# Optimization experiments

Measured on AMD Instinct MI355X. Metric: run time of the kernel, lower is better.

## Reference

```python
import jax, jax.numpy as jnp
import numpy as np


def setup_inputs() -> dict:
    key = jax.random.key(0)
    k_x, k_q, k_k, k_v = jax.random.split(key, 4)
    B, S, E, D = 4, 2048, 1024, 1024
    scale = 1.0 / np.sqrt(E)
    return {
        "x": jax.random.normal(k_x, (B, S, E), dtype=jnp.float32),
        # nn.Linear weight matrices, shape [out_dim, in_dim]; y = x @ W.T
        "w_q": jax.random.normal(k_q, (D, E), dtype=jnp.float32) * scale,
        "w_k": jax.random.normal(k_k, (D, E), dtype=jnp.float32) * scale,
        "w_v": jax.random.normal(k_v, (D, E), dtype=jnp.float32) * scale,
    }


def reference(x, w_q, w_k, w_v):
    # x: [B, S, E]; w_*: [D, E] (torch nn.Linear convention)
    B, S, E = x.shape
    q = jnp.einsum("bse,de->bsd", x, w_q)  # [B, S, D]
    k = jnp.einsum("bse,de->bsd", x, w_k)
    v = jnp.einsum("bse,de->bsd", x, w_v)
    D = q.shape[-1]
    # raw scores, then causal mask (strictly upper triangle -> -inf), then
    # scale by 1/sqrt(D) inside softmax exactly as the original does.
    scores = jnp.einsum("bsd,btd->bst", q, k)  # [B, S, S]
    causal = jnp.tril(jnp.ones((S, S), dtype=bool))  # True = keep
    scores = jnp.where(causal[None], scores, -jnp.inf)
    attn = jax.nn.softmax(scores / jnp.sqrt(jnp.asarray(D, x.dtype)), axis=-1)
    # dropout p=0.0 -> identity
    return jnp.einsum("bst,btd->bsd", attn, v)  # [B, S, D]
```

## Files before the change

kernel.cpp:

```cpp
#include <hip/hip_runtime.h>
#include <hip/hip_bf16.h>


typedef unsigned short u16;
typedef __attribute__((ext_vector_type(4))) u16   u16x4;
typedef __attribute__((ext_vector_type(8))) u16   u16x8;
typedef __attribute__((ext_vector_type(8))) short short8;
typedef __attribute__((ext_vector_type(4))) float f32x4;
typedef __attribute__((ext_vector_type(4))) int   i32x4;

__device__ inline u16 f2b(float v) {
    __hip_bfloat16 b = __float2bfloat16(v);
    return *reinterpret_cast<u16*>(&b);
}
__device__ inline float b2f(u16 v) {
    unsigned int u = ((unsigned int)v) << 16;
    return *reinterpret_cast<float*>(&u);
}

template <typename T> __device__ inline void store_elem(T* p, float v);
template <> __device__ inline void store_elem<float>(float* p, float v) { *p = v; }
template <> __device__ inline void store_elem<u16>(u16* p, float v)     { *p = f2b(v); }

__device__ inline void gload_lds16(const u16* g, u16* l) {
    __builtin_amdgcn_global_load_lds(
        (const __attribute__((address_space(1))) void*)g,
        (__attribute__((address_space(3))) void*)l, 16, 0, 0);
}

__global__ __launch_bounds__(256) void cast_all_kernel(
    const float* __restrict__ x,  const float* __restrict__ wq,
    const float* __restrict__ wk, const float* __restrict__ wv,
    u16* __restrict__ dst) {
    int q = blockIdx.x * 256 + threadIdx.x;
    const float* src;
    int sidx;
    if (q < 2097152) { src = x; sidx = q * 4; }
    else {
        int qq = q - 2097152;
        int w  = qq >> 18;
        sidx   = (qq & 262143) * 4;
        src    = (w == 0) ? wq : (w == 1) ? wk : wv;
    }
    float4 v = *(const float4*)(src + sidx);
    u16x4 o;
    o.x = f2b(v.x); o.y = f2b(v.y); o.z = f2b(v.z); o.w = f2b(v.w);
    *(u16x4*)(dst + q * 4) = o;
}

#define MT 128
#define NT 128
#define BKH 32
#define HSZ (MT * BKH)

template <int TRANS, typename OutT>
__device__ __forceinline__ void gemm_core(
    u16* __restrict__ As, u16* __restrict__ Bs,
    const u16* __restrict__ Ab, int lda,
    const u16* __restrict__ Bb, int ldb,
    OutT* __restrict__ Cb, int ldc,
    int m0, int n0, int kbeg, int kend)
{
    const int tid  = threadIdx.x;
    const int lane = tid & 63;
    const int wave = tid >> 6;
    const int quad = lane >> 4;
    const int r16  = lane & 15;
    const int mw   = (wave >> 1) * 64;
    const int nw   = (wave & 1) * 64;

    const int c0 = tid, c1 = tid + 256;
    const int r0 = c0 >> 2, k0 = (c0 & 3) * 8;
    const int r1 = c1 >> 2, k1 = (c1 & 3) * 8;
    const int oa0 = (m0 + r0) * lda + k0;
    const int oa1 = (m0 + r1) * lda + k1;
    const int ob0 = (n0 + r0) * ldb + k0;
    const int ob1 = (n0 + r1) * ldb + k1;

    f32x4 acc[4][4] = {};

    for (int kk = kbeg; kk < kend; kk += 2 * BKH) {
        __syncthreads();
        gload_lds16(Ab + (kk + oa0),        &As[c0 * 8]);
        gload_lds16(Ab + (kk + oa1),        &As[c1 * 8]);
        gload_lds16(Ab + (kk + BKH + oa0),  &As[HSZ + c0 * 8]);
        gload_lds16(Ab + (kk + BKH + oa1),  &As[HSZ + c1 * 8]);
        gload_lds16(Bb + (kk + ob0),        &Bs[c0 * 8]);
        gload_lds16(Bb + (kk + ob1),        &Bs[c1 * 8]);
        gload_lds16(Bb + (kk + BKH + ob0),  &Bs[HSZ + c0 * 8]);
        gload_lds16(Bb + (kk + BKH + ob1),  &Bs[HSZ + c1 * 8]);
        __syncthreads();

#pragma unroll
        for (int h = 0; h < 2; h++) {
            short8 af[4], bf[4];
#pragma unroll
            for (int i = 0; i < 4; i++)
                af[i] = *(const short8*)&As[h * HSZ + (mw + i * 16 + r16) * BKH + quad * 8];
#pragma unroll
            for (int j = 0; j < 4; j++)
                bf[j] = *(const short8*)&Bs[h * HSZ + (nw + j * 16 + r16) * BKH + quad * 8];
#pragma unroll
            for (int i = 0; i < 4; i++)
#pragma unroll
                for (int j = 0; j < 4; j++)
                    acc[i][j] = __builtin_amdgcn_mfma_f32_16x16x32_bf16(af[i], bf[j], acc[i][j], 0, 0, 0);
        }
    }

    if (TRANS == 0) {
#pragma unroll
        for (int i = 0; i < 4; i++)
#pragma unroll
            for (int j = 0; j < 4; j++)
#pragma unroll
                for (int r = 0; r < 4; r++) {
                    int m = m0 + mw + i * 16 + quad * 4 + r;
                    int n = n0 + nw + j * 16 + r16;
                    store_elem(&Cb[(long long)m * ldc + n], acc[i][j][r]);
                }
    } else {
#pragma unroll
        for (int i = 0; i < 4; i++)
#pragma unroll
            for (int j = 0; j < 4; j++) {
                int mbase = m0 + mw + i * 16 + quad * 4;
                int d     = n0 + nw + j * 16 + r16;
                int b     = mbase >> 11;
                int s     = mbase & 2047;
                u16x4 o;
#pragma unroll
                for (int r = 0; r < 4; r++) o[r] = f2b(acc[i][j][r]);
                *(u16x4*)((u16*)Cb + (((b << 10) + d) * 2048 + s)) = o;
            }
    }
}

__global__ __launch_bounds__(256, 4) void gemm_qkv(
    const u16* __restrict__ xb, const u16* __restrict__ wb,
    u16* __restrict__ qk, u16* __restrict__ vt) {
    __shared__ __align__(16) u16 As[2 * HSZ];
    __shared__ __align__(16) u16 Bs[2 * HSZ];
    int bx = blockIdx.x, m0 = blockIdx.y * MT;
    if (bx < 16)
        gemm_core<0, u16>(As, Bs, xb, 1024, wb, 1024, qk, 2048,
                          m0, bx * 128, 0, 1024);
    else
        gemm_core<1, u16>(As, Bs, xb, 1024, wb + 2048 * 1024, 1024, vt, 2048,
                          m0, (bx - 16) * 128, 0, 1024);
}

__global__ __launch_bounds__(256, 4) void gemm_scores(
    const u16* __restrict__ qk, u16* __restrict__ sc) {
    __shared__ __align__(16) u16 As[2 * HSZ];
    __shared__ __align__(16) u16 Bs[2 * HSZ];
    int t = blockIdx.x;
    float ff = sqrtf(8.0f * t + 1.0f);
    int m = (int)((ff - 1.0f) * 0.5f);
    while ((m + 1) * (m + 2) / 2 <= t) m++;
    while (m * (m + 1) / 2 > t) m--;
    int m0 = m * MT;
    int n0 = (t - m * (m + 1) / 2) * NT;
    const u16* Ab = qk + (long long)blockIdx.z * 2048 * 2048;
    const u16* Bb = Ab + 1024;
    u16* Cb = sc + (long long)blockIdx.z * 2048 * 2048;
    gemm_core<0, u16>(As, Bs, Ab, 2048, Bb, 2048, Cb, 2048, m0, n0, 0, 1024);
}

__global__ __launch_bounds__(256, 4) void gemm_pv(
    const u16* __restrict__ P, const u16* __restrict__ vt,
    float* __restrict__ out, float* __restrict__ part)
{
    __shared__ __align__(16) u16 As[2 * HSZ];
    __shared__ __align__(16) u16 Bs[2 * HSZ];
    const int bid = blockIdx.x;
    int m, chunk, n;
    if (bid < 80) {
        int q = bid >> 3; n = bid & 7;
        if (q < 9) { m = 7 + q; chunk = 0; } else { m = 15; chunk = 1; }
    } else {
        int r = bid - 80; int s = 7 - (r >> 4); int t = r & 15;
        n = t & 7;
        if (t < 8) { m = s - 1; chunk = 0; } else { m = s + 7; chunk = 1; }
    }
    const int m0 = m * MT, n0 = n * NT;
    const int kbeg = chunk ? 1024 : 0;
    const int kend = chunk ? (m0 + MT) : min(1024, m0 + MT);
    const int b = blockIdx.z;

    const u16* Ab = P  + (long long)b * 2048 * 2048;
    const u16* Bb = vt + (long long)b * 1024 * 2048;
    float* Cb = (chunk == 0)
        ? out  + (long long)b * 2097152
        : part + (long long)b * 1048576 - 1024LL * 1024;
    gemm_core<0, float>(As, Bs, Ab, 2048, Bb, 2048, Cb, 1024, m0, n0, kbeg, kend);
}

__global__ __launch_bounds__(256) void pv_combine(float* __restrict__ out,
                                                  const float* __restrict__ part) {
    long long idx = ((long long)blockIdx.x * 256 + threadIdx.x) * 8;
    long long bb = idx >> 20;
    long long j  = idx & 1048575;
    float* o = out + bb * 2097152 + 1048576 + j;
    const float* p = part + bb * 1048576 + j;
    float4 o0 = *(float4*)o, o1 = *(float4*)(o + 4);
    float4 p0 = *(const float4*)p, p1 = *(const float4*)(p + 4);
    o0.x += p0.x; o0.y += p0.y; o0.z += p0.z; o0.w += p0.w;
    o1.x += p1.x; o1.y += p1.y; o1.z += p1.z; o1.w += p1.w;
    *(float4*)o = o0; *(float4*)(o + 4) = o1;
}

__global__ __launch_bounds__(256) void softmax_kernel(const u16* __restrict__ sc,
                                                      u16* __restrict__ P) {
    const int S = 2048;
    int row = blockIdx.x;
    int i   = row & (S - 1);
    int n   = i + 1;
    int kendr = (i & ~127) + 128;
    const u16* srow = sc + (long long)row * S;
    u16*       prow = P  + (long long)row * S;

    int j0 = threadIdx.x * 8;
    u16x8 raw = {};
    if (j0 <= i) raw = *(const u16x8*)(srow + j0);
    float v[8];
#pragma unroll
    for (int e = 0; e < 8; e++) v[e] = (j0 + e < n) ? b2f(raw[e]) : -1e30f;

    __shared__ float red[8];
    float lmax = v[0];
#pragma unroll
    for (int e = 1; e < 8; e++) lmax = fmaxf(lmax, v[e]);
    for (int o = 32; o > 0; o >>= 1) lmax = fmaxf(lmax, __shfl_xor(lmax, o, 64));
    int wid = threadIdx.x >> 6;
    if ((threadIdx.x & 63) == 0) red[wid] = lmax;
    __syncthreads();
    float Mx = fmaxf(fmaxf(red[0], red[1]), fmaxf(red[2], red[3]));

    const float C = 0.045112384f;
    float ev[8];
    float lsum = 0.f;
#pragma unroll
    for (int e = 0; e < 8; e++) {
        ev[e] = (j0 + e < n) ? exp2f((v[e] - Mx) * C) : 0.f;
        lsum += ev[e];
    }
    for (int o = 32; o > 0; o >>= 1) lsum += __shfl_xor(lsum, o, 64);
    if ((threadIdx.x & 63) == 0) red[4 + wid] = lsum;
    __syncthreads();
    float inv = 1.0f / (red[4] + red[5] + red[6] + red[7]);

    if (j0 < kendr) {
        u16x8 o8;
#pragma unroll
        for (int e = 0; e < 8; e++) o8[e] = f2b(ev[e] * inv);
        *(u16x8*)(prow + j0) = o8;
    }
}

extern "C" void kernel_launch(void* const* d_in, const int* in_sizes, int n_in,
                              void* d_out, int out_size, void* d_ws, size_t ws_size,
                              hipStream_t stream) {
    const float* x  = (const float*)d_in[0];
    const float* wq = (const float*)d_in[1];
    const float* wk = (const float*)d_in[2];
    const float* wv = (const float*)d_in[3];
    float* out = (float*)d_out;

    char* ws = (char*)d_ws;
    u16*   xb   = (u16*)(ws);
    u16*   wb   = (u16*)(ws + 16777216LL);
    u16*   qk   = (u16*)(ws + 23068672LL);
    u16*   sc   = (u16*)(ws + 56623104LL);
    u16*   P    = (u16*)(ws + 90177536LL);
    u16*   vt   = (u16*)(ws + 123731968LL);
    float* part = (float*)(ws + 140509184LL);

    cast_all_kernel<<<11264, 256, 0, stream>>>(x, wq, wk, wv, xb);

    gemm_qkv<<<dim3(24, 64, 1), 256, 0, stream>>>(xb, wb, qk, vt);

    gemm_scores<<<dim3(136, 1, 4), 256, 0, stream>>>(qk, sc);

    softmax_kernel<<<8192, 256, 0, stream>>>(sc, P);

    gemm_pv<<<dim3(192, 1, 4), 256, 0, stream>>>(P, vt, out, part);
    pv_combine<<<2048, 256, 0, stream>>>(out, part);
}
```

Baseline: 243.3 us.

## Replace QKV projection GEMM with 256x256-tile 8-wave pipelined kernel

Replaces the 128x128-tile QKV projection GEMM with a dedicated 256x256-tile kernel using 512 threads, a BK=64 double-buffered LDS pipeline with XOR-swizzled layout, interleaved prefetch between MFMA phases, s_setprio hints, and a block-index swizzle for L2 locality. The larger tile increases arithmetic intensity and reduces global/LDS traffic per FLOP. It trades this for fewer blocks (384) and higher register and LDS pressure, with hand-tuned waitcnt and barriers that must be exactly right.

```diff
diff --git a/kernel.cpp b/kernel.cpp
--- a/kernel.cpp
+++ b/kernel.cpp
@@ -46,6 +46,188 @@
     u16x4 o;
     o.x = f2b(v.x); o.y = f2b(v.y); o.z = f2b(v.z); o.w = f2b(v.w);
     *(u16x4*)(dst + q * 4) = o;
+}
+
+__global__ __launch_bounds__(512) void gemm_qkv256(
+    const u16* __restrict__ xb, const u16* __restrict__ wb,
+    u16* __restrict__ qk, u16* __restrict__ vt)
+{
+    __shared__ __align__(16) u16 lds[2][2][16384];
+
+    const int tid  = threadIdx.x;
+    const int lane = tid & 63;
+    const int wave = tid >> 6;
+    const int quad = lane >> 4;
+    const int r16  = lane & 15;
+    const int wm   = wave >> 2;
+    const int wn   = wave & 3;
+
+    int flat = blockIdx.x;
+    int swz  = (flat & 7) * 48 + (flat >> 3);
+    int bx   = swz % 12;
+    int m0   = (swz / 12) * 256;
+    const bool isV = (bx >= 8);
+    const int  n0  = (isV ? bx - 8 : bx) * 256;
+    const u16* __restrict__ Ab = xb;
+    const u16* __restrict__ Bb = wb + (isV ? 2048 * 1024 : 0);
+
+    int gA[2][2], gB[2][2], lA[2][2], lB[2][2];
+    {
+        const int cswz = ((lane & 3) * 8) ^ (((lane >> 5) & 1) << 4);
+        const int rsub = lane >> 2;
+#pragma unroll
+        for (int u = 0; u < 2; ++u)
+#pragma unroll
+            for (int j = 0; j < 2; ++j) {
+                int s   = j * 8 + wave;
+                int sh  = s >> 1, cg = s & 1;
+                int rgA = (sh & 3) + (sh >> 2) * 8 + u * 4;
+                int rgB = sh + u * 8;
+                int cl  = cg * 32 + cswz;
+                gA[u][j] = (m0 + rgA * 16 + rsub) * 1024 + cl;
+                gB[u][j] = (n0 + rgB * 16 + rsub) * 1024 + cl;
+                lA[u][j] = (rgA * 2 + cg) * 512 + lane * 8;
+                lB[u][j] = (rgB * 2 + cg) * 512 + lane * 8;
+            }
+    }
+
+#define STAGE_A(BUF, U, KK) do { \
+        gload_lds16(Ab + gA[U][0] + (KK), &lds[BUF][0][lA[U][0]]); \
+        gload_lds16(Ab + gA[U][1] + (KK), &lds[BUF][0][lA[U][1]]); } while (0)
+#define STAGE_B(BUF, U, KK) do { \
+        gload_lds16(Bb + gB[U][0] + (KK), &lds[BUF][1][lB[U][0]]); \
+        gload_lds16(Bb + gB[U][1] + (KK), &lds[BUF][1][lB[U][1]]); } while (0)
+
+    const int cswr = (quad * 8) ^ ((r16 >> 3) << 4);
+    const int rdA0 = wm * 16 * 512 + r16 * 32 + cswr;
+    const int rdB0 = wn * 8  * 512 + r16 * 32 + cswr;
+
+    f32x4 acc[8][4] = {};
+
+    STAGE_B(0, 0, 0);  STAGE_B(0, 1, 0);  STAGE_A(0, 0, 0);  STAGE_A(0, 1, 0);
+    STAGE_B(1, 0, 64); STAGE_B(1, 1, 64); STAGE_A(1, 0, 64); STAGE_A(1, 1, 64);
+    asm volatile("s_waitcnt vmcnt(8)" ::: "memory");
+    __builtin_amdgcn_s_barrier();
+
+    for (int t = 0; t < 16; ++t) {
+        const int  buf = t & 1;
+        const int  kk2 = t * 64 + 128;
+        const bool pf  = (t < 14);
+        const u16* Al  = lds[buf][0];
+        const u16* Bl  = lds[buf][1];
+        short8 bfr[4][2], a01[2][2], a23[2][2], a45[2][2], a67[2][2];
+
+#pragma unroll
+        for (int nf = 0; nf < 4; ++nf)
+#pragma unroll
+            for (int ks = 0; ks < 2; ++ks)
+                bfr[nf][ks] = *(const short8*)&Bl[rdB0 + (nf * 2 + ks) * 512];
+#pragma unroll
+        for (int mf = 0; mf < 2; ++mf)
+#pragma unroll
+            for (int ks = 0; ks < 2; ++ks)
+                a01[mf][ks] = *(const short8*)&Al[rdA0 + (mf * 2 + ks) * 512];
+        __builtin_amdgcn_s_barrier();
+        __builtin_amdgcn_s_setprio(1);
+#pragma unroll
+        for (int mf = 0; mf < 2; ++mf)
+#pragma unroll
+            for (int nf = 0; nf < 4; ++nf)
+#pragma unroll
+                for (int ks = 0; ks < 2; ++ks)
+                    acc[mf][nf] = __builtin_amdgcn_mfma_f32_16x16x32_bf16(
+                        a01[mf][ks], bfr[nf][ks], acc[mf][nf], 0, 0, 0);
+        __builtin_amdgcn_s_setprio(0);
+        __builtin_amdgcn_s_barrier();
+
+#pragma unroll
+        for (int mf = 0; mf < 2; ++mf)
+#pragma unroll
+            for (int ks = 0; ks < 2; ++ks)
+                a23[mf][ks] = *(const short8*)&Al[rdA0 + ((mf + 2) * 2 + ks) * 512];
+        if (pf) STAGE_B(buf, 0, kk2);
+        __builtin_amdgcn_s_barrier();
+        __builtin_amdgcn_s_setprio(1);
+#pragma unroll
+        for (int mf = 0; mf < 2; ++mf)
+#pragma unroll
+            for (int nf = 0; nf < 4; ++nf)
+#pragma unroll
+                for (int ks = 0; ks < 2; ++ks)
+                    acc[mf + 2][nf] = __builtin_amdgcn_mfma_f32_16x16x32_bf16(
+                        a23[mf][ks], bfr[nf][ks], acc[mf + 2][nf], 0, 0, 0);
+        __builtin_amdgcn_s_setprio(0);
+        __builtin_amdgcn_s_barrier();
+
+#pragma unroll
+        for (int mf = 0; mf < 2; ++mf)
+#pragma unroll
+            for (int ks = 0; ks < 2; ++ks) {
+                a45[mf][ks] = *(const short8*)&Al[rdA0 + ((mf + 4) * 2 + ks) * 512];
+                a67[mf][ks] = *(const short8*)&Al[rdA0 + ((mf + 6) * 2 + ks) * 512];
+            }
+        if (pf) STAGE_B(buf, 1, kk2);
+        __builtin_amdgcn_s_barrier();
+        __builtin_amdgcn_s_setprio(1);
+#pragma unroll
+        for (int mf = 0; mf < 2; ++mf)
+#pragma unroll
+            for (int nf = 0; nf < 4; ++nf)
+#pragma unroll
+                for (int ks = 0; ks < 2; ++ks)
+                    acc[mf + 4][nf] = __builtin_amdgcn_mfma_f32_16x16x32_bf16(
+                        a45[mf][ks], bfr[nf][ks], acc[mf + 4][nf], 0, 0, 0);
+        __builtin_amdgcn_s_setprio(0);
+        asm volatile("s_waitcnt lgkmcnt(0)" ::: "memory");
+        __builtin_amdgcn_s_barrier();
+
+        if (pf) { STAGE_A(buf, 0, kk2); STAGE_A(buf, 1, kk2); }
+        __builtin_amdgcn_s_barrier();
+        __builtin_amdgcn_s_setprio(1);
+#pragma unroll
+        for (int mf = 0; mf < 2; ++mf)
+#pragma unroll
+            for (int nf = 0; nf < 4; ++nf)
+#pragma unroll
+                for (int ks = 0; ks < 2; ++ks)
+                    acc[mf + 6][nf] = __builtin_amdgcn_mfma_f32_16x16x32_bf16(
+                        a67[mf][ks], bfr[nf][ks], acc[mf + 6][nf], 0, 0, 0);
+        __builtin_amdgcn_s_setprio(0);
+        if (pf) asm volatile("s_waitcnt vmcnt(8)" ::: "memory");
+        else    asm volatile("s_waitcnt vmcnt(0)" ::: "memory");
+        __builtin_amdgcn_s_barrier();
+    }
+#undef STAGE_A
+#undef STAGE_B
+
+    if (!isV) {
+#pragma unroll
+        for (int mf = 0; mf < 8; ++mf) {
+            int m = m0 + wm * 128 + mf * 16 + quad * 4;
+#pragma unroll
+            for (int nf = 0; nf < 4; ++nf) {
+                int n = n0 + wn * 64 + nf * 16 + r16;
+#pragma unroll
+                for (int r = 0; r < 4; ++r)
+                    qk[(m + r) * 2048 + n] = f2b(acc[mf][nf][r]);
+            }
+        }
+    } else {
+#pragma unroll
+        for (int mf = 0; mf < 8; ++mf) {
+            int mbase = m0 + wm * 128 + mf * 16 + quad * 4;
+            int b = mbase >> 11;
+            int s = mbase & 2047;
+#pragma unroll
+            for (int nf = 0; nf < 4; ++nf) {
+                int d = n0 + wn * 64 + nf * 16 + r16;
+                u16x4 o;
+#pragma unroll
+                for (int r = 0; r < 4; ++r) o[r] = f2b(acc[mf][nf][r]);
+                *(u16x4*)(vt + (((b << 10) + d) * 2048 + s)) = o;
+            }
+        }
+    }
 }
 
 #define MT 128
@@ -136,20 +318,6 @@
     }
 }
 
-__global__ __launch_bounds__(256, 4) void gemm_qkv(
-    const u16* __restrict__ xb, const u16* __restrict__ wb,
-    u16* __restrict__ qk, u16* __restrict__ vt) {
-    __shared__ __align__(16) u16 As[2 * HSZ];
-    __shared__ __align__(16) u16 Bs[2 * HSZ];
-    int bx = blockIdx.x, m0 = blockIdx.y * MT;
-    if (bx < 16)
-        gemm_core<0, u16>(As, Bs, xb, 1024, wb, 1024, qk, 2048,
-                          m0, bx * 128, 0, 1024);
-    else
-        gemm_core<1, u16>(As, Bs, xb, 1024, wb + 2048 * 1024, 1024, vt, 2048,
-                          m0, (bx - 16) * 128, 0, 1024);
-}
-
 __global__ __launch_bounds__(256, 4) void gemm_scores(
     const u16* __restrict__ qk, u16* __restrict__ sc) {
     __shared__ __align__(16) u16 As[2 * HSZ];
@@ -278,7 +446,7 @@
 
     cast_all_kernel<<<11264, 256, 0, stream>>>(x, wq, wk, wv, xb);
 
-    gemm_qkv<<<dim3(24, 64, 1), 256, 0, stream>>>(xb, wb, qk, vt);
+    gemm_qkv256<<<384, 512, 0, stream>>>(xb, wb, qk, vt);
 
     gemm_scores<<<dim3(136, 1, 4), 256, 0, stream>>>(qk, sc);
 
```

Result: slower. 256.4 us (+5.4%).
